# Optimization experiments

Measured on AMD Instinct MI355X. Metric: run time of the kernel, lower is better.

The kernel has to match this reference:

```python
import jax, jax.numpy as jnp
import numpy as np

N_FEATURES = 512
N_LAYERS = 128
BATCH = 2048
PI = np.pi


def setup_inputs() -> dict:
    key = jax.random.key(0)
    k0, k1, k2, k3, k4 = jax.random.split(key, 5)
    nA = N_FEATURES // 2            # angles per A layer (even pairs)
    nB = (N_FEATURES - 1) // 2      # angles per B layer (odd pairs)
    LB = N_LAYERS // 2
    LA = N_LAYERS - LB              # equal when N_LAYERS even
    return {
        "cmplx": jax.random.normal(k0, (BATCH, N_FEATURES, 2), dtype=jnp.float32),
        "angleA0": jax.random.uniform(k1, (LA, nA), jnp.float32, -PI, PI),
        "angleA1": jax.random.uniform(k2, (LA, nA), jnp.float32, -PI, PI),
        "angleB0": jax.random.uniform(k3, (LB, nB), jnp.float32, -PI, PI),
        "angleB1": jax.random.uniform(k4, (LB, nB), jnp.float32, -PI, PI),
        "omega": jnp.zeros((N_FEATURES,), jnp.float32),
    }


def _mzi(a, b, ang0, ang1):
    # MZI = DC . PS(ang1) . DC . PS(ang0) acting on mode pair (a, b)
    # U = 1/2 [[e^{i phi}(e^{i th}-1),    i(e^{i th}+1)   ],
    #          [i e^{i phi}(e^{i th}+1),  (1 - e^{i th})  ]]
    ephi = jnp.exp(1j * ang0)
    eth = jnp.exp(1j * ang1)
    t = 0.5 * (eth - 1.0)
    u = 0.5 * (eth + 1.0)
    na = ephi * t * a + 1j * u * b
    nb = 1j * ephi * u * a - t * b
    return na, nb


def _layer_A(x, a0, a1):
    # pairs (0,1),(2,3),...
    a = x[:, 0::2]
    b = x[:, 1::2]
    na, nb = _mzi(a, b, a0, a1)
    return jnp.stack([na, nb], axis=-1).reshape(x.shape)


def _layer_B(x, b0, b1):
    # pairs (1,2),(3,4),...; endpoints 0 and N-1 pass through (N even)
    N = x.shape[1]
    a = x[:, 1:N - 1:2]
    b = x[:, 2:N:2]
    na, nb = _mzi(a, b, b0, b1)
    mid = jnp.stack([na, nb], axis=-1).reshape(x.shape[0], N - 2)
    return jnp.concatenate([x[:, :1], mid, x[:, -1:]], axis=1)


def reference(cmplx, angleA0, angleA1, angleB0, angleB1, omega):
    x = cmplx[..., 0] + 1j * cmplx[..., 1]   # [B, N] complex64

    def step(x, angs):
        a0, a1, b0, b1 = angs
        x = _layer_A(x, a0, a1)
        x = _layer_B(x, b0, b1)
        return x, None

    x, _ = jax.lax.scan(step, x, (angleA0, angleA1, angleB0, angleB1))
    out = x * jnp.exp(1j * omega)            # complex diagonal phase
    return jnp.stack([out.real, out.imag], axis=-1)
```

## Files before the change

kernel.cpp:

```cpp
#include <hip/hip_runtime.h>

#define LSTEPS 64
#define NF 512
#define MB 2048
#define CSTRIDE 256

typedef __attribute__((ext_vector_type(8))) short bf16x8;
typedef __attribute__((ext_vector_type(4))) float f32x4;
typedef __attribute__((ext_vector_type(4))) int i32x4;

__device__ __forceinline__ float2 cmul(float2 a, float2 b) {
  return make_float2(fmaf(a.x, b.x, -(a.y * b.y)), fmaf(a.x, b.y, a.y * b.x));
}
__device__ __forceinline__ float2 cfma(float2 a, float2 b, float2 c) {
  return make_float2(fmaf(a.x, b.x, fmaf(-a.y, b.y, c.x)),
                     fmaf(a.x, b.y, fmaf(a.y, b.x, c.y)));
}
__device__ __forceinline__ unsigned short f2bf(float f) {
  union { float f; unsigned u; } v; v.f = f;
  unsigned r = v.u + 0x7FFF + ((v.u >> 16) & 1);
  return (unsigned short)(r >> 16);
}

__global__ __launch_bounds__(256) void prep_kernel(
    const float* __restrict__ a0, const float* __restrict__ a1,
    const float* __restrict__ b0, const float* __restrict__ b1,
    const float4* __restrict__ Xf,
    float4* __restrict__ cA, float4* __restrict__ cB,
    unsigned short* __restrict__ Xr, unsigned short* __restrict__ Xi)
{
  const int bid = blockIdx.x, tid = threadIdx.x;
  if (bid < 64) {
    const int l = bid;
    {
      float ang0 = a0[l * 256 + tid], ang1 = a1[l * 256 + tid];
      float se, ce, st, ct;
      sincosf(ang0, &se, &ce);
      sincosf(ang1, &st, &ct);
      float2 ephi = make_float2(ce, se);
      float2 tt = make_float2(0.5f * (ct - 1.0f), 0.5f * st);
      float2 uu = make_float2(0.5f * (ct + 1.0f), 0.5f * st);
      float2 C1 = cmul(ephi, tt);
      float2 C2 = make_float2(-uu.y, uu.x);
      float2 eu = cmul(ephi, uu);
      float2 C3 = make_float2(-eu.y, eu.x);
      float2 C4 = make_float2(-tt.x, -tt.y);
      float4* dst = cA + (size_t)(l * CSTRIDE + tid) * 2;
      dst[0] = make_float4(C1.x, C1.y, C2.x, C2.y);
      dst[1] = make_float4(C3.x, C3.y, C4.x, C4.y);
    }
    if (tid < 255) {
      float ang0 = b0[l * 255 + tid], ang1 = b1[l * 255 + tid];
      float se, ce, st, ct;
      sincosf(ang0, &se, &ce);
      sincosf(ang1, &st, &ct);
      float2 ephi = make_float2(ce, se);
      float2 tt = make_float2(0.5f * (ct - 1.0f), 0.5f * st);
      float2 uu = make_float2(0.5f * (ct + 1.0f), 0.5f * st);
      float2 C1 = cmul(ephi, tt);
      float2 C2 = make_float2(-uu.y, uu.x);
      float2 eu = cmul(ephi, uu);
      float2 C3 = make_float2(-eu.y, eu.x);
      float2 C4 = make_float2(-tt.x, -tt.y);
      float4* dst = cB + (size_t)(l * CSTRIDE + tid) * 2;
      dst[0] = make_float4(C1.x, C1.y, C2.x, C2.y);
      dst[1] = make_float4(C3.x, C3.y, C4.x, C4.y);
    } else {
      float4* dst = cB + (size_t)(l * CSTRIDE + 255) * 2;
      dst[0] = make_float4(0.f, 0.f, 0.f, 0.f);
      dst[1] = make_float4(0.f, 0.f, 0.f, 0.f);
    }
  } else {
    const int qi = (bid - 64) * 256 + tid;
    float4 v0 = Xf[(size_t)qi * 2];
    float4 v1 = Xf[(size_t)qi * 2 + 1];
    ushort4 r, im;
    r.x = f2bf(v0.x); im.x = f2bf(v0.y);
    r.y = f2bf(v0.z); im.y = f2bf(v0.w);
    r.z = f2bf(v1.x); im.z = f2bf(v1.y);
    r.w = f2bf(v1.z); im.w = f2bf(v1.w);
    *(ushort4*)(Xr + (size_t)qi * 4) = r;
    *(ushort4*)(Xi + (size_t)qi * 4) = im;
  }
}

struct MZS { float2 a0, b0, a1, b1; };

__device__ __forceinline__ void mzi_apply(const float4& k0, const float4& k1,
                                          float2& a, float2& b) {
  float2 c1 = make_float2(k0.x, k0.y), c2 = make_float2(k0.z, k0.w);
  float2 c3 = make_float2(k1.x, k1.y), c4 = make_float2(k1.z, k1.w);
  float2 na = cfma(c2, b, cmul(c1, a));
  float2 nb = cfma(c4, b, cmul(c3, a));
  a = na; b = nb;
}
__device__ __forceinline__ float2 mzi_bnd(const float4& k0, const float4& k1,
                                          float2& a, float2 b, bool en) {
  float2 d1 = make_float2(k0.x, k0.y), d2 = make_float2(k0.z, k0.w);
  float2 d3 = make_float2(k1.x, k1.y), d4 = make_float2(k1.z, k1.w);
  float2 na = cfma(d2, b, cmul(d1, a));
  float2 nb = cfma(d4, b, cmul(d3, a));
  if (en) a = na;
  return en ? nb : make_float2(0.f, 0.f);
}

__device__ __forceinline__ void load_bank(float4 (&K)[8],
    const float4* __restrict__ cA, const float4* __restrict__ cB, int l, int q0)
{
  const float4* pa = cA + (size_t)l * (CSTRIDE * 2) + (size_t)q0 * 2;
  const float4* pb = cB + (size_t)l * (CSTRIDE * 2) + (size_t)q0 * 2;
  K[0] = pa[0]; K[1] = pa[1]; K[2] = pa[2]; K[3] = pa[3];
  K[4] = pb[0]; K[5] = pb[1]; K[6] = pb[2]; K[7] = pb[3];
}

__device__ __forceinline__ void step_state(const float4 (&K)[8], int L, bool hasBnd,
                                           MZS& s)
{
  mzi_apply(K[0], K[1], s.a0, s.b0);
  mzi_apply(K[2], K[3], s.a1, s.b1);
  float xnx = __shfl_down(s.a0.x, 1);
  float xny = __shfl_down(s.a0.y, 1);
  float2 xn = (L == 63) ? make_float2(0.f, 0.f) : make_float2(xnx, xny);
  float2 nbo = mzi_bnd(K[6], K[7], s.b1, xn, hasBnd);
  mzi_apply(K[4], K[5], s.b0, s.a1);
  float px = __shfl_up(nbo.x, 1);
  float py = __shfl_up(nbo.y, 1);
  if (L > 0) s.a0 = make_float2(px, py);
}

__global__ __launch_bounds__(64, 1) void mesh_kernel(
    const float4* __restrict__ cA, const float4* __restrict__ cB,
    unsigned short* __restrict__ Ur, unsigned short* __restrict__ Ui)
{
  const int bid = blockIdx.x;
  const int c = (bid & 7) * 32 + (bid >> 3);
  const int L = threadIdx.x;
  int ws = c - 63; ws = ws < 0 ? 0 : (ws > 128 ? 128 : ws);
  const int q0 = ws + 2 * L, q1 = q0 + 1;
  const bool hasBnd = (q1 < 255);

  MZS s0, s1;
  s0.a0 = make_float2((q0 == c) ? 1.f : 0.f, 0.f);
  s0.b0 = make_float2(0.f, 0.f);
  s0.a1 = make_float2((q1 == c) ? 1.f : 0.f, 0.f);
  s0.b1 = make_float2(0.f, 0.f);
  s1.a0 = make_float2(0.f, 0.f);
  s1.b0 = make_float2((q0 == c) ? 1.f : 0.f, 0.f);
  s1.a1 = make_float2(0.f, 0.f);
  s1.b1 = make_float2((q1 == c) ? 1.f : 0.f, 0.f);

  float4 K0[8], K1[8], K2[8];
  load_bank(K0, cA, cB, 0, q0);
  load_bank(K1, cA, cB, 1, q0);
  load_bank(K2, cA, cB, 2, q0);

#pragma unroll 1
  for (int l = 0; l < 63; l += 3) {
    step_state(K0, L, hasBnd, s0); step_state(K0, L, hasBnd, s1);
    load_bank(K0, cA, cB, (l + 3 < 64) ? l + 3 : 63, q0);
    step_state(K1, L, hasBnd, s0); step_state(K1, L, hasBnd, s1);
    load_bank(K1, cA, cB, (l + 4 < 64) ? l + 4 : 63, q0);
    step_state(K2, L, hasBnd, s0); step_state(K2, L, hasBnd, s1);
    load_bank(K2, cA, cB, (l + 5 < 64) ? l + 5 : 63, q0);
  }
  step_state(K0, L, hasBnd, s0); step_state(K0, L, hasBnd, s1);

  unsigned* Ur32 = (unsigned*)Ur;
  unsigned* Ui32 = (unsigned*)Ui;
  const int rows[4] = {2 * q0, 2 * q0 + 1, 2 * q1, 2 * q1 + 1};
  const float2 v0[4] = {s0.a0, s0.b0, s0.a1, s0.b1};
  const float2 v1[4] = {s1.a0, s1.b0, s1.a1, s1.b1};
#pragma unroll
  for (int e = 0; e < 4; ++e) {
    unsigned pr = (unsigned)f2bf(v0[e].x) | ((unsigned)f2bf(v1[e].x) << 16);
    unsigned pi = (unsigned)f2bf(v0[e].y) | ((unsigned)f2bf(v1[e].y) << 16);
    Ur32[(size_t)rows[e] * (NF / 2) + c] = pr;
    Ui32[(size_t)rows[e] * (NF / 2) + c] = pi;
  }
#pragma unroll
  for (int e = 0; e < 4; ++e) {
    const int row = (2 * ws + 256 + 4 * L + e) & 511;
    Ur32[(size_t)row * (NF / 2) + c] = 0u;
    Ui32[(size_t)row * (NF / 2) + c] = 0u;
  }
}

#define BMT 32
#define BNT 64
#define LDT 72

__global__ __launch_bounds__(256) void cgemm_kernel(
    const unsigned short* __restrict__ Xr, const unsigned short* __restrict__ Xi,
    const unsigned short* __restrict__ Ur, const unsigned short* __restrict__ Ui,
    const float* __restrict__ omega,
    float2* __restrict__ Y)
{
  __shared__ __align__(16) unsigned short Ars[BMT][LDT];
  __shared__ __align__(16) unsigned short Ais[BMT][LDT];
  __shared__ __align__(16) unsigned short Brs[BNT][LDT];
  __shared__ __align__(16) unsigned short Bis[BNT][LDT];

  const int tid = threadIdx.x;
  const int w = tid >> 6;
  const int wm = w & 1;
  const int wn = w >> 1;
  const int lane = tid & 63;
  const int bm = (blockIdx.x >> 3) * BMT;
  const int bn = (blockIdx.x & 7) * BNT;

  int klo = bn - 132; klo = klo < 0 ? 0 : klo; klo &= ~63;
  int khi = bn + 196; khi = khi > NF ? NF : khi; khi = (khi + 63) & ~63;

  f32x4 acc_r[2], acc_i[2];
#pragma unroll
  for (int nf = 0; nf < 2; ++nf) {
    acc_r[nf] = (f32x4){0.f, 0.f, 0.f, 0.f};
    acc_i[nf] = (f32x4){0.f, 0.f, 0.f, 0.f};
  }

  const int sar = tid >> 3, sak = (tid & 7) * 8;
  const int sbr = tid >> 2, sbk = (tid & 3) * 16;

  for (int k0 = klo; k0 < khi; k0 += 64) {
    const uint4* gar = (const uint4*)(Xr + (size_t)(bm + sar) * NF + k0 + sak);
    const uint4* gai = (const uint4*)(Xi + (size_t)(bm + sar) * NF + k0 + sak);
    const uint4* gbr = (const uint4*)(Ur + (size_t)(bn + sbr) * NF + k0 + sbk);
    const uint4* gbi = (const uint4*)(Ui + (size_t)(bn + sbr) * NF + k0 + sbk);
    uint4 ar = gar[0];
    uint4 ai = gai[0];
    uint4 br0 = gbr[0], br1 = gbr[1];
    uint4 bi0 = gbi[0], bi1 = gbi[1];

    if (k0 > klo) __syncthreads();

    *(uint4*)&Ars[sar][sak]     = ar;
    *(uint4*)&Ais[sar][sak]     = ai;
    *(uint4*)&Brs[sbr][sbk]     = br0;
    *(uint4*)&Brs[sbr][sbk + 8] = br1;
    *(uint4*)&Bis[sbr][sbk]     = bi0;
    *(uint4*)&Bis[sbr][sbk + 8] = bi1;

    __syncthreads();

#pragma unroll
    for (int kk = 0; kk < 2; ++kk) {
      const int ko = kk * 32 + (lane >> 4) * 8;
      bf16x8 afr = *(const bf16x8*)&Ars[wm * 16 + (lane & 15)][ko];
      bf16x8 afi = *(const bf16x8*)&Ais[wm * 16 + (lane & 15)][ko];
      i32x4 neg = (i32x4)afi ^ (int)0x80008000;
      bf16x8 afin = (bf16x8)neg;
#pragma unroll
      for (int nf = 0; nf < 2; ++nf) {
        bf16x8 bfr = *(const bf16x8*)&Brs[wn * 32 + nf * 16 + (lane & 15)][ko];
        bf16x8 bfi = *(const bf16x8*)&Bis[wn * 32 + nf * 16 + (lane & 15)][ko];
        acc_r[nf] = __builtin_amdgcn_mfma_f32_16x16x32_bf16(afr,  bfr, acc_r[nf], 0, 0, 0);
        acc_r[nf] = __builtin_amdgcn_mfma_f32_16x16x32_bf16(afin, bfi, acc_r[nf], 0, 0, 0);
        acc_i[nf] = __builtin_amdgcn_mfma_f32_16x16x32_bf16(afr,  bfi, acc_i[nf], 0, 0, 0);
        acc_i[nf] = __builtin_amdgcn_mfma_f32_16x16x32_bf16(afi,  bfr, acc_i[nf], 0, 0, 0);
      }
    }
  }

  const int dn0 = bn + wn * 32 + (lane & 15);
  const int dm0 = bm + wm * 16 + (lane >> 4) * 4;
#pragma unroll
  for (int nf = 0; nf < 2; ++nf) {
    const int n = dn0 + nf * 16;
    float sn, cn;
    sincosf(omega[n], &sn, &cn);
#pragma unroll
    for (int r = 0; r < 4; ++r) {
      float yr = acc_r[nf][r], yi = acc_i[nf][r];
      Y[(size_t)(dm0 + r) * NF + n] =
          make_float2(fmaf(yr, cn, -(yi * sn)), fmaf(yr, sn, yi * cn));
    }
  }
}

extern "C" void kernel_launch(void* const* d_in, const int* in_sizes, int n_in,
                              void* d_out, int out_size, void* d_ws, size_t ws_size,
                              hipStream_t stream) {
  const float* cmplx = (const float*)d_in[0];
  const float* a0    = (const float*)d_in[1];
  const float* a1    = (const float*)d_in[2];
  const float* b0    = (const float*)d_in[3];
  const float* b1    = (const float*)d_in[4];
  const float* omega = (const float*)d_in[5];

  size_t off = 0;
  float4* cA = (float4*)((char*)d_ws + off); off += (size_t)LSTEPS * CSTRIDE * 2 * sizeof(float4);
  float4* cB = (float4*)((char*)d_ws + off); off += (size_t)LSTEPS * CSTRIDE * 2 * sizeof(float4);
  unsigned short* Ur = (unsigned short*)((char*)d_ws + off); off += (size_t)NF * NF * 2;
  unsigned short* Ui = (unsigned short*)((char*)d_ws + off); off += (size_t)NF * NF * 2;
  unsigned short* Xr = (unsigned short*)((char*)d_ws + off); off += (size_t)MB * NF * 2;
  unsigned short* Xi = (unsigned short*)((char*)d_ws + off); off += (size_t)MB * NF * 2;

  prep_kernel<<<1088, 256, 0, stream>>>(a0, a1, b0, b1, (const float4*)cmplx,
                                        cA, cB, Xr, Xi);
  mesh_kernel<<<256, 64, 0, stream>>>(cA, cB, Ur, Ui);
  cgemm_kernel<<<(MB / BMT) * (NF / BNT), 256, 0, stream>>>(
      Xr, Xi, Ur, Ui, omega, (float2*)d_out);
}
```

Before: 50.25 us.

## Split mesh into four layer chunks and chain banded complex GEMMs

The serial 64-step mesh construction is replaced by four independent 16-step chunk matrices built in parallel across 1024 blocks. The input is then multiplied through four chained banded complex GEMMs, with a narrower K band per chunk, writing bf16 intermediates between stages. This cuts the serial depth and latency of building the unitary. In exchange it adds three kernel launches, more total GEMM traffic through intermediate buffers, and extra bf16 rounding between stages, which may hurt accuracy.

```diff
diff --git a/kernel.cpp b/kernel.cpp
--- a/kernel.cpp
+++ b/kernel.cpp
@@ -4,6 +4,8 @@
 #define NF 512
 #define MB 2048
 #define CSTRIDE 256
+#define PL (NF * NF)
+#define LDT 72
 
 typedef __attribute__((ext_vector_type(8))) short bf16x8;
 typedef __attribute__((ext_vector_type(4))) float f32x4;
@@ -103,7 +105,6 @@
   if (en) a = na;
   return en ? nb : make_float2(0.f, 0.f);
 }
-
 __device__ __forceinline__ void load_bank(float4 (&K)[8],
     const float4* __restrict__ cA, const float4* __restrict__ cB, int l, int q0)
 {
@@ -112,7 +113,6 @@
   K[0] = pa[0]; K[1] = pa[1]; K[2] = pa[2]; K[3] = pa[3];
   K[4] = pb[0]; K[5] = pb[1]; K[6] = pb[2]; K[7] = pb[3];
 }
-
 __device__ __forceinline__ void step_state(const float4 (&K)[8], int L, bool hasBnd,
                                            MZS& s)
 {
@@ -128,12 +128,14 @@
   if (L > 0) s.a0 = make_float2(px, py);
 }
 
-__global__ __launch_bounds__(64, 1) void mesh_kernel(
+__global__ __launch_bounds__(64) void chunk_mesh(
     const float4* __restrict__ cA, const float4* __restrict__ cB,
-    unsigned short* __restrict__ Ur, unsigned short* __restrict__ Ui)
+    unsigned short* __restrict__ Cb)
 {
   const int bid = blockIdx.x;
-  const int c = (bid & 7) * 32 + (bid >> 3);
+  const int m = bid >> 8;
+  const int cb = bid & 255;
+  const int c = (cb & 7) * 32 + (cb >> 3);
   const int L = threadIdx.x;
   int ws = c - 63; ws = ws < 0 ? 0 : (ws > 128 ? 128 : ws);
   const int q0 = ws + 2 * L, q1 = q0 + 1;
@@ -149,24 +151,22 @@
   s1.a1 = make_float2(0.f, 0.f);
   s1.b1 = make_float2((q1 == c) ? 1.f : 0.f, 0.f);
 
-  float4 K0[8], K1[8], K2[8];
-  load_bank(K0, cA, cB, 0, q0);
-  load_bank(K1, cA, cB, 1, q0);
-  load_bank(K2, cA, cB, 2, q0);
-
+  const int l0 = m * 16;
+  float4 K0[8], K1[8];
+  load_bank(K0, cA, cB, l0 + 0, q0);
+  load_bank(K1, cA, cB, l0 + 1, q0);
 #pragma unroll 1
-  for (int l = 0; l < 63; l += 3) {
+  for (int i = 0; i < 14; i += 2) {
     step_state(K0, L, hasBnd, s0); step_state(K0, L, hasBnd, s1);
-    load_bank(K0, cA, cB, (l + 3 < 64) ? l + 3 : 63, q0);
+    load_bank(K0, cA, cB, l0 + ((i + 2 < 16) ? i + 2 : 15), q0);
     step_state(K1, L, hasBnd, s0); step_state(K1, L, hasBnd, s1);
-    load_bank(K1, cA, cB, (l + 4 < 64) ? l + 4 : 63, q0);
-    step_state(K2, L, hasBnd, s0); step_state(K2, L, hasBnd, s1);
-    load_bank(K2, cA, cB, (l + 5 < 64) ? l + 5 : 63, q0);
+    load_bank(K1, cA, cB, l0 + ((i + 3 < 16) ? i + 3 : 15), q0);
   }
   step_state(K0, L, hasBnd, s0); step_state(K0, L, hasBnd, s1);
-
-  unsigned* Ur32 = (unsigned*)Ur;
-  unsigned* Ui32 = (unsigned*)Ui;
+  step_state(K1, L, hasBnd, s0); step_state(K1, L, hasBnd, s1);
+
+  unsigned* nr32 = (unsigned*)(Cb + (size_t)m * 2 * PL);
+  unsigned* ni32 = nr32 + PL / 2;
   const int rows[4] = {2 * q0, 2 * q0 + 1, 2 * q1, 2 * q1 + 1};
   const float2 v0[4] = {s0.a0, s0.b0, s0.a1, s0.b1};
   const float2 v1[4] = {s1.a0, s1.b0, s1.a1, s1.b1};
@@ -174,42 +174,37 @@
   for (int e = 0; e < 4; ++e) {
     unsigned pr = (unsigned)f2bf(v0[e].x) | ((unsigned)f2bf(v1[e].x) << 16);
     unsigned pi = (unsigned)f2bf(v0[e].y) | ((unsigned)f2bf(v1[e].y) << 16);
-    Ur32[(size_t)rows[e] * (NF / 2) + c] = pr;
-    Ui32[(size_t)rows[e] * (NF / 2) + c] = pi;
+    nr32[(size_t)rows[e] * (NF / 2) + c] = pr;
+    ni32[(size_t)rows[e] * (NF / 2) + c] = pi;
   }
 #pragma unroll
   for (int e = 0; e < 4; ++e) {
     const int row = (2 * ws + 256 + 4 * L + e) & 511;
-    Ur32[(size_t)row * (NF / 2) + c] = 0u;
-    Ui32[(size_t)row * (NF / 2) + c] = 0u;
-  }
-}
-
-#define BMT 32
-#define BNT 64
-#define LDT 72
-
-__global__ __launch_bounds__(256) void cgemm_kernel(
-    const unsigned short* __restrict__ Xr, const unsigned short* __restrict__ Xi,
-    const unsigned short* __restrict__ Ur, const unsigned short* __restrict__ Ui,
-    const float* __restrict__ omega,
-    float2* __restrict__ Y)
-{
-  __shared__ __align__(16) unsigned short Ars[BMT][LDT];
-  __shared__ __align__(16) unsigned short Ais[BMT][LDT];
-  __shared__ __align__(16) unsigned short Brs[BNT][LDT];
-  __shared__ __align__(16) unsigned short Bis[BNT][LDT];
+    nr32[(size_t)row * (NF / 2) + c] = 0u;
+    ni32[(size_t)row * (NF / 2) + c] = 0u;
+  }
+}
+
+template <bool FINAL>
+__global__ __launch_bounds__(256) void gemm_kernel(
+    const unsigned short* __restrict__ Zr, const unsigned short* __restrict__ Zi,
+    const unsigned short* __restrict__ Cr, const unsigned short* __restrict__ Ci,
+    unsigned short* __restrict__ Or, unsigned short* __restrict__ Oi,
+    const float* __restrict__ omega, float2* __restrict__ Y)
+{
+  __shared__ __align__(16) unsigned short Ars[32][LDT];
+  __shared__ __align__(16) unsigned short Ais[32][LDT];
+  __shared__ __align__(16) unsigned short Brs[64][LDT];
+  __shared__ __align__(16) unsigned short Bis[64][LDT];
 
   const int tid = threadIdx.x;
-  const int w = tid >> 6;
-  const int wm = w & 1;
-  const int wn = w >> 1;
+  const int w = tid >> 6, wm = w & 1, wn = w >> 1;
   const int lane = tid & 63;
-  const int bm = (blockIdx.x >> 3) * BMT;
-  const int bn = (blockIdx.x & 7) * BNT;
-
-  int klo = bn - 132; klo = klo < 0 ? 0 : klo; klo &= ~63;
-  int khi = bn + 196; khi = khi > NF ? NF : khi; khi = (khi + 63) & ~63;
+  const int bm = (blockIdx.x >> 3) * 32;
+  const int bn = (blockIdx.x & 7) * 64;
+
+  int klo = bn - 40; if (klo < 0) klo = 0; klo &= ~63;
+  int khi = bn + 104; if (khi > NF) khi = NF; khi = (khi + 63) & ~63;
 
   f32x4 acc_r[2], acc_i[2];
 #pragma unroll
@@ -217,15 +212,14 @@
     acc_r[nf] = (f32x4){0.f, 0.f, 0.f, 0.f};
     acc_i[nf] = (f32x4){0.f, 0.f, 0.f, 0.f};
   }
-
   const int sar = tid >> 3, sak = (tid & 7) * 8;
   const int sbr = tid >> 2, sbk = (tid & 3) * 16;
 
   for (int k0 = klo; k0 < khi; k0 += 64) {
-    const uint4* gar = (const uint4*)(Xr + (size_t)(bm + sar) * NF + k0 + sak);
-    const uint4* gai = (const uint4*)(Xi + (size_t)(bm + sar) * NF + k0 + sak);
-    const uint4* gbr = (const uint4*)(Ur + (size_t)(bn + sbr) * NF + k0 + sbk);
-    const uint4* gbi = (const uint4*)(Ui + (size_t)(bn + sbr) * NF + k0 + sbk);
+    const uint4* gar = (const uint4*)(Zr + (size_t)(bm + sar) * NF + k0 + sak);
+    const uint4* gai = (const uint4*)(Zi + (size_t)(bm + sar) * NF + k0 + sak);
+    const uint4* gbr = (const uint4*)(Cr + (size_t)(bn + sbr) * NF + k0 + sbk);
+    const uint4* gbi = (const uint4*)(Ci + (size_t)(bn + sbr) * NF + k0 + sbk);
     uint4 ar = gar[0];
     uint4 ai = gai[0];
     uint4 br0 = gbr[0], br1 = gbr[1];
@@ -266,13 +260,21 @@
 #pragma unroll
   for (int nf = 0; nf < 2; ++nf) {
     const int n = dn0 + nf * 16;
-    float sn, cn;
-    sincosf(omega[n], &sn, &cn);
-#pragma unroll
-    for (int r = 0; r < 4; ++r) {
-      float yr = acc_r[nf][r], yi = acc_i[nf][r];
-      Y[(size_t)(dm0 + r) * NF + n] =
-          make_float2(fmaf(yr, cn, -(yi * sn)), fmaf(yr, sn, yi * cn));
+    if (FINAL) {
+      float sn, cn;
+      sincosf(omega[n], &sn, &cn);
+#pragma unroll
+      for (int r = 0; r < 4; ++r) {
+        float yr = acc_r[nf][r], yi = acc_i[nf][r];
+        Y[(size_t)(dm0 + r) * NF + n] =
+            make_float2(fmaf(yr, cn, -(yi * sn)), fmaf(yr, sn, yi * cn));
+      }
+    } else {
+#pragma unroll
+      for (int r = 0; r < 4; ++r) {
+        Or[(size_t)(dm0 + r) * NF + n] = f2bf(acc_r[nf][r]);
+        Oi[(size_t)(dm0 + r) * NF + n] = f2bf(acc_i[nf][r]);
+      }
     }
   }
 }
@@ -290,14 +292,27 @@
   size_t off = 0;
   float4* cA = (float4*)((char*)d_ws + off); off += (size_t)LSTEPS * CSTRIDE * 2 * sizeof(float4);
   float4* cB = (float4*)((char*)d_ws + off); off += (size_t)LSTEPS * CSTRIDE * 2 * sizeof(float4);
-  unsigned short* Ur = (unsigned short*)((char*)d_ws + off); off += (size_t)NF * NF * 2;
-  unsigned short* Ui = (unsigned short*)((char*)d_ws + off); off += (size_t)NF * NF * 2;
   unsigned short* Xr = (unsigned short*)((char*)d_ws + off); off += (size_t)MB * NF * 2;
   unsigned short* Xi = (unsigned short*)((char*)d_ws + off); off += (size_t)MB * NF * 2;
+  unsigned short* Cb = (unsigned short*)((char*)d_ws + off); off += (size_t)4 * 2 * PL * 2;
+  unsigned short* Z1r = (unsigned short*)((char*)d_ws + off); off += (size_t)MB * NF * 2;
+  unsigned short* Z1i = (unsigned short*)((char*)d_ws + off); off += (size_t)MB * NF * 2;
+  unsigned short* Z2r = (unsigned short*)((char*)d_ws + off); off += (size_t)MB * NF * 2;
+  unsigned short* Z2i = (unsigned short*)((char*)d_ws + off); off += (size_t)MB * NF * 2;
+  float2* Y = (float2*)d_out;
 
   prep_kernel<<<1088, 256, 0, stream>>>(a0, a1, b0, b1, (const float4*)cmplx,
                                         cA, cB, Xr, Xi);
-  mesh_kernel<<<256, 64, 0, stream>>>(cA, cB, Ur, Ui);
-  cgemm_kernel<<<(MB / BMT) * (NF / BNT), 256, 0, stream>>>(
-      Xr, Xi, Ur, Ui, omega, (float2*)d_out);
-}
+  chunk_mesh<<<1024, 64, 0, stream>>>(cA, cB, Cb);
+
+  const unsigned short* C0r = Cb;               const unsigned short* C0i = Cb + PL;
+  const unsigned short* C1r = Cb + 2 * PL;      const unsigned short* C1i = Cb + 3 * PL;
+  const unsigned short* C2r = Cb + 4 * PL;      const unsigned short* C2i = Cb + 5 * PL;
+  const unsigned short* C3r = Cb + 6 * PL;      const unsigned short* C3i = Cb + 7 * PL;
+
+  const int grid = (MB / 32) * (NF / 64);
+  gemm_kernel<false><<<grid, 256, 0, stream>>>(Xr,  Xi,  C0r, C0i, Z1r, Z1i, omega, Y);
+  gemm_kernel<false><<<grid, 256, 0, stream>>>(Z1r, Z1i, C1r, C1i, Z2r, Z2i, omega, Y);
+  gemm_kernel<false><<<grid, 256, 0, stream>>>(Z2r, Z2i, C2r, C2i, Z1r, Z1i, omega, Y);
+  gemm_kernel<true> <<<grid, 256, 0, stream>>>(Z1r, Z1i, C3r, C3i, Z2r, Z2i, omega, Y);
+}
```

After: 51.08 us. No clear change (+1.6%).
